# Kernel tuning notes

Hardware: AMD Instinct MI355X
Metric: run time of the kernel (lower is better)

Reference implementation:

```python
import jax, jax.numpy as jnp
import numpy as np

STATE_BITS = 10          # L: bits of trellis state
SHIFT_BITS = 2           # K: bits shifted in per step -> 2^K predecessors
CHUNK = 4                # chunk_size: values emitted per trellis step
S = 1 << STATE_BITS      # number of states (codebook rows)
NPRED = 1 << SHIFT_BITS  # predecessors per state
HI = 1 << (STATE_BITS - SHIFT_BITS)


def setup_inputs() -> dict:
    key = jax.random.key(0)
    k1, k2 = jax.random.split(key)
    array = jax.random.normal(k1, (1024, 1024), dtype=jnp.float32)
    codebook = jax.random.normal(k2, (S, CHUNK), dtype=jnp.float32)
    return {"array": array, "codebook": codebook, "block_size": 16}


def _viterbi(x, codebook):
    # x: [T, CHUNK, B] target chunks; codebook: [S, CHUNK]
    # Exact min-squared-error Viterbi over the bit-shift trellis:
    #   next_state = ((prev << K) | new_bits) mod 2^L
    # Predecessors of state s: (s >> K) + j * 2^(L-K), j in [0, 2^K)
    s = jnp.arange(S)
    prev_idx = (s[:, None] >> SHIFT_BITS) + jnp.arange(NPRED)[None, :] * HI  # [S, NPRED]
    cnorm = jnp.sum(codebook * codebook, axis=1)  # [S]

    def cost(xt):  # xt: [CHUNK, B] -> [S, B] squared distances
        return cnorm[:, None] - 2.0 * (codebook @ xt) + jnp.sum(xt * xt, axis=0)[None, :]

    alpha0 = cost(x[0])  # free initial state: cost of emitting first chunk

    def step(alpha, xt):
        cand = alpha[prev_idx]                        # [S, NPRED, B]
        j = jnp.argmin(cand, axis=1)                  # [S, B]
        alpha_new = jnp.min(cand, axis=1) + cost(xt)  # [S, B]
        return alpha_new, j.astype(jnp.int8)

    alpha_T, bps = jax.lax.scan(step, alpha0, x[1:])  # bps: [T-1, S, B] int8
    last = jnp.argmin(alpha_T, axis=0).astype(jnp.int32)  # [B] state at step T-1

    def back(state, bp):
        # state: [B] state at step t; bp: [S, B] backpointers into step t
        j = jnp.take_along_axis(bp, state[None, :], axis=0)[0].astype(jnp.int32)
        prev = (state >> SHIFT_BITS) + j * HI
        return prev, state

    first, rest = jax.lax.scan(back, last, bps, reverse=True)
    return jnp.concatenate([first[None], rest], axis=0)  # [T, B] int32


def reference(array, codebook, block_size):
    rows, columns = array.shape
    br, bc = rows // block_size, columns // block_size
    epb = block_size * block_size          # elements_per_block
    T = epb // CHUNK                       # number_of_steps
    B = br * bc                            # number_of_blocks
    # block reshape: [rows, cols] -> [elements_per_block, number_of_blocks]
    blocks = (array.reshape(br, block_size, bc, block_size)
                   .transpose(0, 2, 1, 3)
                   .reshape(B, epb).T)
    x = blocks.reshape(T, CHUNK, B)
    states = _viterbi(x, codebook)         # [T, B]
    vals = codebook[states]                # [T, B, CHUNK] gather reconstruct
    rec = vals.transpose(0, 2, 1).reshape(epb, B)
    rec = (rec.T.reshape(br, bc, block_size, block_size)
              .transpose(0, 2, 1, 3)
              .reshape(rows, columns))
    states_out = states.T.reshape(br, bc, T)
    return rec, states_out
```

## Files before the change

kernel.cpp:

```cpp
#include <hip/hip_runtime.h>


#define COLS      1024
#define T_STEPS   64
#define REC_SIZE  (1024 * 1024)

__global__ __launch_bounds__(256) void viterbi_q(
    const float* __restrict__ arr,
    const float* __restrict__ cbook,
    float* __restrict__ out)
{
    const int tid   = threadIdx.x;
    const int wid   = tid >> 6;
    const int lane  = tid & 63;
    const int chain = (blockIdx.x << 2) | wid;
    const int rb    = chain >> 6;
    const int cb    = chain & 63;

    __shared__ __align__(16) float tile[4][256];
    __shared__ __align__(16) float Mst[4][256];
    __shared__ unsigned char Jb[4][63 * 64];
    __shared__ int st_lds[4][64];

    {
        const int r  = lane >> 2;
        const int c4 = (lane & 3) << 2;
        float4 v = *(const float4*)(arr + (rb * 16 + r) * COLS + cb * 16 + c4);
        *(float4*)&tile[wid][lane << 2] = v;
    }
    *(float4*)&Mst[wid][lane << 2] = make_float4(0.f, 0.f, 0.f, 0.f);

    float4 a[16];
    float  nrm[16];
    #pragma unroll
    for (int j = 0; j < 4; ++j) {
        #pragma unroll
        for (int c = 0; c < 4; ++c) {
            const int row = (lane << 2) + c + (j << 8);
            float4 v = *(const float4*)(cbook + row * 4);
            nrm[j * 4 + c] = v.x * v.x + v.y * v.y + v.z * v.z + v.w * v.w;
            a[j * 4 + c]   = make_float4(-2.f * v.x, -2.f * v.y,
                                         -2.f * v.z, -2.f * v.w);
        }
    }

    for (int t = 0; t < T_STEPS - 1; ++t) {
        float4 xt = *(const float4*)&tile[wid][t << 2];
        const float xn = xt.x * xt.x + xt.y * xt.y + xt.z * xt.z + xt.w * xt.w;
        float mj[4];
        #pragma unroll
        for (int j = 0; j < 4; ++j)
            mj[j] = Mst[wid][lane + 64 * j] + xn;

        float nm[4];
        unsigned bp = 0;
        #pragma unroll
        for (int c = 0; c < 4; ++c) {
            float cand[4];
            #pragma unroll
            for (int j = 0; j < 4; ++j) {
                float acc = nrm[j * 4 + c] + mj[j];
                const float4 av = a[j * 4 + c];
                acc = fmaf(av.x, xt.x, acc);
                acc = fmaf(av.y, xt.y, acc);
                acc = fmaf(av.z, xt.z, acc);
                acc = fmaf(av.w, xt.w, acc);
                cand[j] = acc;
            }
            const float v = fminf(fminf(cand[0], cand[1]),
                                  fminf(cand[2], cand[3]));
            const int j = (cand[0] == v) ? 0
                        : (cand[1] == v) ? 1
                        : (cand[2] == v) ? 2 : 3;
            nm[c] = v;
            bp |= (unsigned)j << (2 * c);
        }
        *(float4*)&Mst[wid][lane << 2] = make_float4(nm[0], nm[1], nm[2], nm[3]);
        Jb[wid][t * 64 + lane] = (unsigned char)bp;
    }

    int bests;
    {
        const int t = T_STEPS - 1;
        float4 xt = *(const float4*)&tile[wid][t << 2];
        const float xn = xt.x * xt.x + xt.y * xt.y + xt.z * xt.z + xt.w * xt.w;
        float mj[4];
        #pragma unroll
        for (int j = 0; j < 4; ++j)
            mj[j] = Mst[wid][lane + 64 * j] + xn;

        float bv = 3.4e38f;
        int   bs = 0;
        #pragma unroll
        for (int j = 0; j < 4; ++j) {
            #pragma unroll
            for (int c = 0; c < 4; ++c) {
                float acc = nrm[j * 4 + c] + mj[j];
                const float4 av = a[j * 4 + c];
                acc = fmaf(av.x, xt.x, acc);
                acc = fmaf(av.y, xt.y, acc);
                acc = fmaf(av.z, xt.z, acc);
                acc = fmaf(av.w, xt.w, acc);
                if (acc < bv) { bv = acc; bs = (lane << 2) + c + (j << 8); }
            }
        }
        #pragma unroll
        for (int off = 32; off > 0; off >>= 1) {
            const float ov = __shfl_xor(bv, off, 64);
            const int   os = __shfl_xor(bs, off, 64);
            if (ov < bv || (ov == bv && os < bs)) { bv = ov; bs = os; }
        }
        bests = bs;
    }

    if (lane == 0) {
        int s = bests;
        st_lds[wid][T_STEPS - 1] = s;
        for (int i = T_STEPS - 2; i >= 0; --i) {
            const int p = s >> 2;
            const unsigned byte = Jb[wid][i * 64 + (p >> 2)];
            const int j = (byte >> (2 * (p & 3))) & 3;
            s = p + (j << 8);
            st_lds[wid][i] = s;
        }
    }
    __syncthreads();

    const int st = st_lds[wid][lane];
    out[REC_SIZE + chain * 64 + lane] = (float)st;
    const float4 v = *(const float4*)(cbook + st * 4);
    const int r  = lane >> 2;
    const int c4 = (lane & 3) << 2;
    *(float4*)(out + (rb * 16 + r) * COLS + cb * 16 + c4) = v;
}

extern "C" void kernel_launch(void* const* d_in, const int* in_sizes, int n_in,
                              void* d_out, int out_size, void* d_ws, size_t ws_size,
                              hipStream_t stream)
{
    const float* arr   = (const float*)d_in[0];
    const float* cbook = (const float*)d_in[1];
    float* out = (float*)d_out;
    viterbi_q<<<dim3(1024), dim3(256), 0, stream>>>(arr, cbook, out);
}
```

Measured before the change: 120.9 us.

## Rewrite forward Viterbi loop in inline asm with packed FMA and max-form costs

Replaces the compiler-generated forward recursion with a hand-written GCN assembly loop that keeps the codebook in fixed VGPRs. It uses v_pk_fma_f32 on a duplicated input tile to compute two candidate costs per instruction. The cost is rewritten as a maximisation of x·c - 0.5|c|^2 minus accumulated error, which drops the per-step |x|^2 term and the -2 scaling. Blocks shrink to one 64-thread wave each, launched 4096 times. The risks are fragile hard-coded register allocation inside inline asm, a changed tie-breaking order, and different floating-point rounding compared with the reference.

```diff
diff --git a/kernel.cpp b/kernel.cpp
--- a/kernel.cpp
+++ b/kernel.cpp
@@ -5,133 +5,325 @@
 #define T_STEPS   64
 #define REC_SIZE  (1024 * 1024)
 
-__global__ __launch_bounds__(256) void viterbi_q(
+__global__ __launch_bounds__(64) void viterbi_q(
     const float* __restrict__ arr,
     const float* __restrict__ cbook,
     float* __restrict__ out)
 {
-    const int tid   = threadIdx.x;
-    const int wid   = tid >> 6;
-    const int lane  = tid & 63;
-    const int chain = (blockIdx.x << 2) | wid;
+    const int lane  = threadIdx.x;
+    const int chain = blockIdx.x;
     const int rb    = chain >> 6;
-    const int cb    = chain & 63;
-
-    __shared__ __align__(16) float tile[4][256];
-    __shared__ __align__(16) float Mst[4][256];
-    __shared__ unsigned char Jb[4][63 * 64];
-    __shared__ int st_lds[4][64];
+    const int cbc   = chain & 63;
+
+    __shared__ __align__(16) float tile2[512];
+    __shared__ __align__(16) float Msh[256];
+    __shared__ unsigned char Jsh[63 * 64];
+    __shared__ int st_lds[64];
 
     {
         const int r  = lane >> 2;
         const int c4 = (lane & 3) << 2;
-        float4 v = *(const float4*)(arr + (rb * 16 + r) * COLS + cb * 16 + c4);
-        *(float4*)&tile[wid][lane << 2] = v;
+        float4 v = *(const float4*)(arr + (rb * 16 + r) * COLS + cbc * 16 + c4);
+        *(float4*)&tile2[lane * 8]     = make_float4(v.x, v.x, v.y, v.y);
+        *(float4*)&tile2[lane * 8 + 4] = make_float4(v.z, v.z, v.w, v.w);
     }
-    *(float4*)&Mst[wid][lane << 2] = make_float4(0.f, 0.f, 0.f, 0.f);
-
-    float4 a[16];
-    float  nrm[16];
-    #pragma unroll
-    for (int j = 0; j < 4; ++j) {
-        #pragma unroll
-        for (int c = 0; c < 4; ++c) {
-            const int row = (lane << 2) + c + (j << 8);
-            float4 v = *(const float4*)(cbook + row * 4);
-            nrm[j * 4 + c] = v.x * v.x + v.y * v.y + v.z * v.z + v.w * v.w;
-            a[j * 4 + c]   = make_float4(-2.f * v.x, -2.f * v.y,
-                                         -2.f * v.z, -2.f * v.w);
-        }
-    }
-
-    for (int t = 0; t < T_STEPS - 1; ++t) {
-        float4 xt = *(const float4*)&tile[wid][t << 2];
-        const float xn = xt.x * xt.x + xt.y * xt.y + xt.z * xt.z + xt.w * xt.w;
+
+    const unsigned t_off  = (unsigned)(uintptr_t)&tile2[0];
+    const unsigned j_off  = (unsigned)(uintptr_t)&Jsh[0] + lane;
+    const unsigned mr_off = (unsigned)(uintptr_t)&Msh[0] + lane * 4;
+    const unsigned mw_off = (unsigned)(uintptr_t)&Msh[0] + lane * 16;
+    const unsigned g_off  = (unsigned)(lane * 64);
+
+    asm volatile(
+        "s_waitcnt lgkmcnt(0)\n"
+        "v_mov_b32 v22, %[vt]\n"
+        "v_mov_b32 v23, %[vj]\n"
+        "v_mov_b32 v124, %[go]\n"
+        "global_load_dwordx4 v[64:67], v124, %[cbp]\n"
+        "global_load_dwordx4 v[68:71], v124, %[cbp] offset:16\n"
+        "v_add_u32 v124, 0x1000, v124\n"
+        "global_load_dwordx4 v[72:75], v124, %[cbp]\n"
+        "global_load_dwordx4 v[76:79], v124, %[cbp] offset:16\n"
+        "v_add_u32 v124, 0x1000, v124\n"
+        "global_load_dwordx4 v[80:83], v124, %[cbp]\n"
+        "global_load_dwordx4 v[84:87], v124, %[cbp] offset:16\n"
+        "v_add_u32 v124, 0x1000, v124\n"
+        "global_load_dwordx4 v[88:91], v124, %[cbp]\n"
+        "global_load_dwordx4 v[92:95], v124, %[cbp] offset:16\n"
+        "v_add_u32 v124, 0xffffd020, v124\n"
+        "global_load_dwordx4 v[96:99], v124, %[cbp]\n"
+        "global_load_dwordx4 v[100:103], v124, %[cbp] offset:16\n"
+        "v_add_u32 v124, 0x1000, v124\n"
+        "global_load_dwordx4 v[104:107], v124, %[cbp]\n"
+        "global_load_dwordx4 v[108:111], v124, %[cbp] offset:16\n"
+        "v_add_u32 v124, 0x1000, v124\n"
+        "global_load_dwordx4 v[112:115], v124, %[cbp]\n"
+        "global_load_dwordx4 v[116:119], v124, %[cbp] offset:16\n"
+        "v_add_u32 v124, 0x1000, v124\n"
+        "global_load_dwordx4 v[120:123], v124, %[cbp]\n"
+        "global_load_dwordx4 v[124:127], v124, %[cbp] offset:16\n"
+        "s_waitcnt vmcnt(0)\n"
+        "v_mov_b32 v24, v64\n"  "v_mov_b32 v25, v68\n"
+        "v_mov_b32 v26, v65\n"  "v_mov_b32 v27, v69\n"
+        "v_mov_b32 v28, v66\n"  "v_mov_b32 v29, v70\n"
+        "v_mov_b32 v30, v67\n"  "v_mov_b32 v31, v71\n"
+        "v_mul_f32 v32, v64, v64\n" "v_fmac_f32 v32, v65, v65\n"
+        "v_fmac_f32 v32, v66, v66\n" "v_fmac_f32 v32, v67, v67\n"
+        "v_mul_f32 v32, -0.5, v32\n"
+        "v_mul_f32 v33, v68, v68\n" "v_fmac_f32 v33, v69, v69\n"
+        "v_fmac_f32 v33, v70, v70\n" "v_fmac_f32 v33, v71, v71\n"
+        "v_mul_f32 v33, -0.5, v33\n"
+        "v_mov_b32 v34, v72\n"  "v_mov_b32 v35, v76\n"
+        "v_mov_b32 v36, v73\n"  "v_mov_b32 v37, v77\n"
+        "v_mov_b32 v38, v74\n"  "v_mov_b32 v39, v78\n"
+        "v_mov_b32 v40, v75\n"  "v_mov_b32 v41, v79\n"
+        "v_mul_f32 v42, v72, v72\n" "v_fmac_f32 v42, v73, v73\n"
+        "v_fmac_f32 v42, v74, v74\n" "v_fmac_f32 v42, v75, v75\n"
+        "v_mul_f32 v42, -0.5, v42\n"
+        "v_mul_f32 v43, v76, v76\n" "v_fmac_f32 v43, v77, v77\n"
+        "v_fmac_f32 v43, v78, v78\n" "v_fmac_f32 v43, v79, v79\n"
+        "v_mul_f32 v43, -0.5, v43\n"
+        "v_mov_b32 v44, v80\n"  "v_mov_b32 v45, v84\n"
+        "v_mov_b32 v46, v81\n"  "v_mov_b32 v47, v85\n"
+        "v_mov_b32 v48, v82\n"  "v_mov_b32 v49, v86\n"
+        "v_mov_b32 v50, v83\n"  "v_mov_b32 v51, v87\n"
+        "v_mul_f32 v52, v80, v80\n" "v_fmac_f32 v52, v81, v81\n"
+        "v_fmac_f32 v52, v82, v82\n" "v_fmac_f32 v52, v83, v83\n"
+        "v_mul_f32 v52, -0.5, v52\n"
+        "v_mul_f32 v53, v84, v84\n" "v_fmac_f32 v53, v85, v85\n"
+        "v_fmac_f32 v53, v86, v86\n" "v_fmac_f32 v53, v87, v87\n"
+        "v_mul_f32 v53, -0.5, v53\n"
+        "v_mov_b32 v54, v88\n"  "v_mov_b32 v55, v92\n"
+        "v_mov_b32 v56, v89\n"  "v_mov_b32 v57, v93\n"
+        "v_mov_b32 v58, v90\n"  "v_mov_b32 v59, v94\n"
+        "v_mov_b32 v60, v91\n"  "v_mov_b32 v61, v95\n"
+        "v_mul_f32 v62, v88, v88\n" "v_fmac_f32 v62, v89, v89\n"
+        "v_fmac_f32 v62, v90, v90\n" "v_fmac_f32 v62, v91, v91\n"
+        "v_mul_f32 v62, -0.5, v62\n"
+        "v_mul_f32 v63, v92, v92\n" "v_fmac_f32 v63, v93, v93\n"
+        "v_fmac_f32 v63, v94, v94\n" "v_fmac_f32 v63, v95, v95\n"
+        "v_mul_f32 v63, -0.5, v63\n"
+        "v_mov_b32 v64, v96\n"   "v_mov_b32 v65, v100\n"
+        "v_mov_b32 v66, v97\n"   "v_mov_b32 v67, v101\n"
+        "v_mov_b32 v68, v98\n"   "v_mov_b32 v69, v102\n"
+        "v_mov_b32 v70, v99\n"   "v_mov_b32 v71, v103\n"
+        "v_mul_f32 v72, v96, v96\n"  "v_fmac_f32 v72, v97, v97\n"
+        "v_fmac_f32 v72, v98, v98\n" "v_fmac_f32 v72, v99, v99\n"
+        "v_mul_f32 v72, -0.5, v72\n"
+        "v_mul_f32 v73, v100, v100\n" "v_fmac_f32 v73, v101, v101\n"
+        "v_fmac_f32 v73, v102, v102\n" "v_fmac_f32 v73, v103, v103\n"
+        "v_mul_f32 v73, -0.5, v73\n"
+        "v_mov_b32 v74, v104\n"  "v_mov_b32 v75, v108\n"
+        "v_mov_b32 v76, v105\n"  "v_mov_b32 v77, v109\n"
+        "v_mov_b32 v78, v106\n"  "v_mov_b32 v79, v110\n"
+        "v_mov_b32 v80, v107\n"  "v_mov_b32 v81, v111\n"
+        "v_mul_f32 v82, v104, v104\n" "v_fmac_f32 v82, v105, v105\n"
+        "v_fmac_f32 v82, v106, v106\n" "v_fmac_f32 v82, v107, v107\n"
+        "v_mul_f32 v82, -0.5, v82\n"
+        "v_mul_f32 v83, v108, v108\n" "v_fmac_f32 v83, v109, v109\n"
+        "v_fmac_f32 v83, v110, v110\n" "v_fmac_f32 v83, v111, v111\n"
+        "v_mul_f32 v83, -0.5, v83\n"
+        "v_mov_b32 v84, v112\n"  "v_mov_b32 v85, v116\n"
+        "v_mov_b32 v86, v113\n"  "v_mov_b32 v87, v117\n"
+        "v_mov_b32 v88, v114\n"  "v_mov_b32 v89, v118\n"
+        "v_mov_b32 v90, v115\n"  "v_mov_b32 v91, v119\n"
+        "v_mul_f32 v92, v112, v112\n" "v_fmac_f32 v92, v113, v113\n"
+        "v_fmac_f32 v92, v114, v114\n" "v_fmac_f32 v92, v115, v115\n"
+        "v_mul_f32 v92, -0.5, v92\n"
+        "v_mul_f32 v93, v116, v116\n" "v_fmac_f32 v93, v117, v117\n"
+        "v_fmac_f32 v93, v118, v118\n" "v_fmac_f32 v93, v119, v119\n"
+        "v_mul_f32 v93, -0.5, v93\n"
+        "v_mov_b32 v94, v120\n"  "v_mov_b32 v95, v124\n"
+        "v_mov_b32 v96, v121\n"  "v_mov_b32 v97, v125\n"
+        "v_mov_b32 v98, v122\n"  "v_mov_b32 v99, v126\n"
+        "v_mov_b32 v100, v123\n" "v_mov_b32 v101, v127\n"
+        "v_mul_f32 v102, v120, v120\n" "v_fmac_f32 v102, v121, v121\n"
+        "v_fmac_f32 v102, v122, v122\n" "v_fmac_f32 v102, v123, v123\n"
+        "v_mul_f32 v102, -0.5, v102\n"
+        "v_mul_f32 v103, v124, v124\n" "v_fmac_f32 v103, v125, v125\n"
+        "v_fmac_f32 v103, v126, v126\n" "v_fmac_f32 v103, v127, v127\n"
+        "v_mul_f32 v103, -0.5, v103\n"
+        "v_mov_b32 v126, %[mr]\n"
+        "v_mov_b32 v127, %[mw]\n"
+        "v_mov_b32 v116, 0\n" "v_mov_b32 v117, 0\n"
+        "v_mov_b32 v118, 0\n" "v_mov_b32 v119, 0\n"
+        "ds_write_b128 v127, v[116:119]\n"
+        "s_movk_i32 s20, 63\n"
+        "L_fwd_%=:\n"
+        "ds_read_b128 v[104:107], v22\n"
+        "ds_read_b128 v[108:111], v22 offset:16\n"
+        "ds_read2_b32 v[112:113], v126 offset0:0 offset1:64\n"
+        "ds_read2_b32 v[114:115], v126 offset0:128 offset1:192\n"
+        "s_waitcnt lgkmcnt(2)\n"
+        "v_pk_fma_f32 v[116:117], v[24:25], v[104:105], v[32:33]\n"
+        "v_pk_fma_f32 v[118:119], v[64:65], v[104:105], v[72:73]\n"
+        "v_pk_fma_f32 v[116:117], v[26:27], v[106:107], v[116:117]\n"
+        "v_pk_fma_f32 v[118:119], v[66:67], v[106:107], v[118:119]\n"
+        "v_pk_fma_f32 v[116:117], v[28:29], v[108:109], v[116:117]\n"
+        "v_pk_fma_f32 v[118:119], v[68:69], v[108:109], v[118:119]\n"
+        "v_pk_fma_f32 v[116:117], v[30:31], v[110:111], v[116:117]\n"
+        "v_pk_fma_f32 v[118:119], v[70:71], v[110:111], v[118:119]\n"
+        "s_waitcnt lgkmcnt(0)\n"
+        "v_add_f32 v116, v112, v116\n"
+        "v_add_f32 v117, v112, v117\n"
+        "v_add_f32 v118, v112, v118\n"
+        "v_add_f32 v119, v112, v119\n"
+        "v_pk_fma_f32 v[124:125], v[34:35], v[104:105], v[42:43]\n"
+        "v_pk_fma_f32 v[124:125], v[36:37], v[106:107], v[124:125]\n"
+        "v_pk_fma_f32 v[124:125], v[38:39], v[108:109], v[124:125]\n"
+        "v_pk_fma_f32 v[124:125], v[40:41], v[110:111], v[124:125]\n"
+        "v_add_f32 v124, v113, v124\n"
+        "v_add_f32 v125, v113, v125\n"
+        "v_cmp_gt_f32 vcc, v124, v116\n"
+        "v_cndmask_b32 v120, 0, 1, vcc\n"
+        "v_max_f32 v116, v116, v124\n"
+        "v_cmp_gt_f32 vcc, v125, v117\n"
+        "v_cndmask_b32 v121, 0, 1, vcc\n"
+        "v_max_f32 v117, v117, v125\n"
+        "v_pk_fma_f32 v[124:125], v[74:75], v[104:105], v[82:83]\n"
+        "v_pk_fma_f32 v[124:125], v[76:77], v[106:107], v[124:125]\n"
+        "v_pk_fma_f32 v[124:125], v[78:79], v[108:109], v[124:125]\n"
+        "v_pk_fma_f32 v[124:125], v[80:81], v[110:111], v[124:125]\n"
+        "v_add_f32 v124, v113, v124\n"
+        "v_add_f32 v125, v113, v125\n"
+        "v_cmp_gt_f32 vcc, v124, v118\n"
+        "v_cndmask_b32 v122, 0, 1, vcc\n"
+        "v_max_f32 v118, v118, v124\n"
+        "v_cmp_gt_f32 vcc, v125, v119\n"
+        "v_cndmask_b32 v123, 0, 1, vcc\n"
+        "v_max_f32 v119, v119, v125\n"
+        "v_pk_fma_f32 v[124:125], v[44:45], v[104:105], v[52:53]\n"
+        "v_pk_fma_f32 v[124:125], v[46:47], v[106:107], v[124:125]\n"
+        "v_pk_fma_f32 v[124:125], v[48:49], v[108:109], v[124:125]\n"
+        "v_pk_fma_f32 v[124:125], v[50:51], v[110:111], v[124:125]\n"
+        "v_add_f32 v124, v114, v124\n"
+        "v_add_f32 v125, v114, v125\n"
+        "v_cmp_gt_f32 vcc, v124, v116\n"
+        "v_cndmask_b32 v120, v120, 2, vcc\n"
+        "v_max_f32 v116, v116, v124\n"
+        "v_cmp_gt_f32 vcc, v125, v117\n"
+        "v_cndmask_b32 v121, v121, 2, vcc\n"
+        "v_max_f32 v117, v117, v125\n"
+        "v_pk_fma_f32 v[124:125], v[84:85], v[104:105], v[92:93]\n"
+        "v_pk_fma_f32 v[124:125], v[86:87], v[106:107], v[124:125]\n"
+        "v_pk_fma_f32 v[124:125], v[88:89], v[108:109], v[124:125]\n"
+        "v_pk_fma_f32 v[124:125], v[90:91], v[110:111], v[124:125]\n"
+        "v_add_f32 v124, v114, v124\n"
+        "v_add_f32 v125, v114, v125\n"
+        "v_cmp_gt_f32 vcc, v124, v118\n"
+        "v_cndmask_b32 v122, v122, 2, vcc\n"
+        "v_max_f32 v118, v118, v124\n"
+        "v_cmp_gt_f32 vcc, v125, v119\n"
+        "v_cndmask_b32 v123, v123, 2, vcc\n"
+        "v_max_f32 v119, v119, v125\n"
+        "v_pk_fma_f32 v[124:125], v[54:55], v[104:105], v[62:63]\n"
+        "v_pk_fma_f32 v[124:125], v[56:57], v[106:107], v[124:125]\n"
+        "v_pk_fma_f32 v[124:125], v[58:59], v[108:109], v[124:125]\n"
+        "v_pk_fma_f32 v[124:125], v[60:61], v[110:111], v[124:125]\n"
+        "v_add_f32 v124, v115, v124\n"
+        "v_add_f32 v125, v115, v125\n"
+        "v_cmp_gt_f32 vcc, v124, v116\n"
+        "v_cndmask_b32 v120, v120, 3, vcc\n"
+        "v_max_f32 v116, v116, v124\n"
+        "v_cmp_gt_f32 vcc, v125, v117\n"
+        "v_cndmask_b32 v121, v121, 3, vcc\n"
+        "v_max_f32 v117, v117, v125\n"
+        "v_pk_fma_f32 v[124:125], v[94:95], v[104:105], v[102:103]\n"
+        "v_pk_fma_f32 v[124:125], v[96:97], v[106:107], v[124:125]\n"
+        "v_pk_fma_f32 v[124:125], v[98:99], v[108:109], v[124:125]\n"
+        "v_pk_fma_f32 v[124:125], v[100:101], v[110:111], v[124:125]\n"
+        "v_add_f32 v124, v115, v124\n"
+        "v_add_f32 v125, v115, v125\n"
+        "v_cmp_gt_f32 vcc, v124, v118\n"
+        "v_cndmask_b32 v122, v122, 3, vcc\n"
+        "v_max_f32 v118, v118, v124\n"
+        "v_cmp_gt_f32 vcc, v125, v119\n"
+        "v_cndmask_b32 v123, v123, 3, vcc\n"
+        "v_max_f32 v119, v119, v125\n"
+        "v_lshlrev_b32 v124, 2, v121\n"
+        "v_or_b32 v120, v120, v124\n"
+        "v_lshlrev_b32 v124, 4, v122\n"
+        "v_or_b32 v120, v120, v124\n"
+        "v_lshlrev_b32 v124, 6, v123\n"
+        "v_or_b32 v120, v120, v124\n"
+        "ds_write_b128 v127, v[116:119]\n"
+        "ds_write_b8 v23, v120\n"
+        "v_add_u32 v22, 32, v22\n"
+        "v_add_u32 v23, 64, v23\n"
+        "s_waitcnt lgkmcnt(0)\n"
+        "s_sub_u32 s20, s20, 1\n"
+        "s_cmp_lg_u32 s20, 0\n"
+        "s_cbranch_scc1 L_fwd_%=\n"
+        :
+        : [vt] "v"(t_off), [vj] "v"(j_off), [mr] "v"(mr_off),
+          [mw] "v"(mw_off), [go] "v"(g_off), [cbp] "s"(cbook)
+        : "memory", "vcc", "scc", "s20",
+          "v22","v23","v24","v25","v26","v27","v28","v29","v30","v31",
+          "v32","v33","v34","v35","v36","v37","v38","v39","v40","v41",
+          "v42","v43","v44","v45","v46","v47","v48","v49","v50","v51",
+          "v52","v53","v54","v55","v56","v57","v58","v59","v60","v61",
+          "v62","v63","v64","v65","v66","v67","v68","v69","v70","v71",
+          "v72","v73","v74","v75","v76","v77","v78","v79","v80","v81",
+          "v82","v83","v84","v85","v86","v87","v88","v89","v90","v91",
+          "v92","v93","v94","v95","v96","v97","v98","v99","v100","v101",
+          "v102","v103","v104","v105","v106","v107","v108","v109","v110","v111",
+          "v112","v113","v114","v115","v116","v117","v118","v119","v120","v121",
+          "v122","v123","v124","v125","v126","v127");
+
+    int bests;
+    {
+        const float x0 = tile2[504], y0 = tile2[506],
+                    z0 = tile2[508], w0 = tile2[510];
         float mj[4];
         #pragma unroll
-        for (int j = 0; j < 4; ++j)
-            mj[j] = Mst[wid][lane + 64 * j] + xn;
-
-        float nm[4];
-        unsigned bp = 0;
-        #pragma unroll
-        for (int c = 0; c < 4; ++c) {
-            float cand[4];
-            #pragma unroll
-            for (int j = 0; j < 4; ++j) {
-                float acc = nrm[j * 4 + c] + mj[j];
-                const float4 av = a[j * 4 + c];
-                acc = fmaf(av.x, xt.x, acc);
-                acc = fmaf(av.y, xt.y, acc);
-                acc = fmaf(av.z, xt.z, acc);
-                acc = fmaf(av.w, xt.w, acc);
-                cand[j] = acc;
-            }
-            const float v = fminf(fminf(cand[0], cand[1]),
-                                  fminf(cand[2], cand[3]));
-            const int j = (cand[0] == v) ? 0
-                        : (cand[1] == v) ? 1
-                        : (cand[2] == v) ? 2 : 3;
-            nm[c] = v;
-            bp |= (unsigned)j << (2 * c);
-        }
-        *(float4*)&Mst[wid][lane << 2] = make_float4(nm[0], nm[1], nm[2], nm[3]);
-        Jb[wid][t * 64 + lane] = (unsigned char)bp;
-    }
-
-    int bests;
-    {
-        const int t = T_STEPS - 1;
-        float4 xt = *(const float4*)&tile[wid][t << 2];
-        const float xn = xt.x * xt.x + xt.y * xt.y + xt.z * xt.z + xt.w * xt.w;
-        float mj[4];
-        #pragma unroll
-        for (int j = 0; j < 4; ++j)
-            mj[j] = Mst[wid][lane + 64 * j] + xn;
-
-        float bv = 3.4e38f;
+        for (int j = 0; j < 4; ++j) mj[j] = Msh[lane + 64 * j];
+
+        float bv = -3.4e38f;
         int   bs = 0;
         #pragma unroll
         for (int j = 0; j < 4; ++j) {
             #pragma unroll
             for (int c = 0; c < 4; ++c) {
-                float acc = nrm[j * 4 + c] + mj[j];
-                const float4 av = a[j * 4 + c];
-                acc = fmaf(av.x, xt.x, acc);
-                acc = fmaf(av.y, xt.y, acc);
-                acc = fmaf(av.z, xt.z, acc);
-                acc = fmaf(av.w, xt.w, acc);
-                if (acc < bv) { bv = acc; bs = (lane << 2) + c + (j << 8); }
+                const int row = 4 * lane + c + (j << 8);
+                float4 v = *(const float4*)(cbook + row * 4);
+                float h = -0.5f * (v.x * v.x + v.y * v.y +
+                                   v.z * v.z + v.w * v.w);
+                float acc = fmaf(v.x, x0, h);
+                acc = fmaf(v.y, y0, acc);
+                acc = fmaf(v.z, z0, acc);
+                acc = fmaf(v.w, w0, acc);
+                acc += mj[j];
+                if (acc > bv) { bv = acc; bs = row; }
             }
         }
         #pragma unroll
         for (int off = 32; off > 0; off >>= 1) {
             const float ov = __shfl_xor(bv, off, 64);
             const int   os = __shfl_xor(bs, off, 64);
-            if (ov < bv || (ov == bv && os < bs)) { bv = ov; bs = os; }
+            if (ov > bv || (ov == bv && os < bs)) { bv = ov; bs = os; }
         }
         bests = bs;
     }
 
     if (lane == 0) {
         int s = bests;
-        st_lds[wid][T_STEPS - 1] = s;
+        st_lds[T_STEPS - 1] = s;
         for (int i = T_STEPS - 2; i >= 0; --i) {
             const int p = s >> 2;
-            const unsigned byte = Jb[wid][i * 64 + (p >> 2)];
+            const unsigned byte = Jsh[i * 64 + (p >> 2)];
             const int j = (byte >> (2 * (p & 3))) & 3;
             s = p + (j << 8);
-            st_lds[wid][i] = s;
+            st_lds[i] = s;
         }
     }
     __syncthreads();
 
-    const int st = st_lds[wid][lane];
+    const int st = st_lds[lane];
     out[REC_SIZE + chain * 64 + lane] = (float)st;
     const float4 v = *(const float4*)(cbook + st * 4);
     const int r  = lane >> 2;
     const int c4 = (lane & 3) << 2;
-    *(float4*)(out + (rb * 16 + r) * COLS + cb * 16 + c4) = v;
+    *(float4*)(out + (rb * 16 + r) * COLS + cbc * 16 + c4) = v;
 }
 
 extern "C" void kernel_launch(void* const* d_in, const int* in_sizes, int n_in,
@@ -141,5 +333,5 @@
     const float* arr   = (const float*)d_in[0];
     const float* cbook = (const float*)d_in[1];
     float* out = (float*)d_out;
-    viterbi_q<<<dim3(1024), dim3(256), 0, stream>>>(arr, cbook, out);
+    viterbi_q<<<dim3(4096), dim3(64), 0, stream>>>(arr, cbook, out);
 }
```

After: 112.0 us. 7.4% less time.
